# Performance work log

Measured on AMD Instinct MI355X. Metric: run time of the kernel, lower is better.

The kernel has to match this reference:

```python
import jax, jax.numpy as jnp
import numpy as np

SEQ_LEN, BATCH, HID, INP = 512, 256, 256, 256


def setup_inputs() -> dict:
    key = jax.random.key(0)
    ks = jax.random.split(key, 6)
    s = 1.0 / np.sqrt(HID)  # torch GRUCell init scale
    return {
        "carry": jnp.zeros((BATCH, HID), jnp.float32),
        "seq_inputs": jax.random.normal(ks[0], (SEQ_LEN, BATCH, INP), jnp.float32),
        "seq_resets": jax.random.randint(ks[1], (SEQ_LEN, BATCH), 0, 2, jnp.int32),
        "w_ih": jax.random.uniform(ks[2], (3 * HID, INP), jnp.float32, -s, s),
        "w_hh": jax.random.uniform(ks[3], (3 * HID, HID), jnp.float32, -s, s),
        "b_ih": jax.random.uniform(ks[4], (3 * HID,), jnp.float32, -s, s),
        "b_hh": jax.random.uniform(ks[5], (3 * HID,), jnp.float32, -s, s),
    }


def reference(carry, seq_inputs, seq_resets, w_ih, w_hh, b_ih, b_hh):
    # Precompute the input-side projection for all timesteps in one GEMM.
    gi_all = jnp.einsum('tbi,gi->tbg', seq_inputs, w_ih) + b_ih  # (T,B,3H)

    def step(h, xs):
        gi, reset_t = xs
        h = jnp.where(reset_t[:, None] > 0, jnp.zeros_like(h), h)
        gh = h @ w_hh.T + b_hh  # (B,3H)
        i_r, i_z, i_n = jnp.split(gi, 3, axis=1)
        h_r, h_z, h_n = jnp.split(gh, 3, axis=1)
        r = jax.nn.sigmoid(i_r + h_r)
        z = jax.nn.sigmoid(i_z + h_z)
        n = jnp.tanh(i_n + r * h_n)
        h_new = (1.0 - z) * n + z * h
        return h_new, h_new

    h_final, outputs = jax.lax.scan(step, carry, (gi_all, seq_resets))
    return h_final, outputs
```

## Files before the change

### kernel.cpp

```cpp
#include <hip/hip_runtime.h>
#include <hip/hip_bf16.h>
#include <hip/hip_fp16.h>


#define T_LEN 512
#define BATCH 256
#define HID   256

typedef __attribute__((ext_vector_type(8))) short s16x8;
typedef __attribute__((ext_vector_type(4))) float fx4;
typedef __attribute__((ext_vector_type(4))) unsigned short u16x4;

#define MFMA16 __builtin_amdgcn_mfma_f32_16x16x32_bf16

#define GATE_STRIDE 4096u
#define BLK_STRIDE  12288u
#define T_STRIDE    196608u

__device__ __forceinline__ unsigned short f2bf(float f) {
  union { float f; unsigned u; } v; v.f = f;
  unsigned r = v.u + 0x7fffu + ((v.u >> 16) & 1u);
  return (unsigned short)(r >> 16);
}

__device__ __forceinline__ s16x8 pack8(float4 a, float4 b) {
  s16x8 f;
  f[0] = (short)f2bf(a.x); f[1] = (short)f2bf(a.y);
  f[2] = (short)f2bf(a.z); f[3] = (short)f2bf(a.w);
  f[4] = (short)f2bf(b.x); f[5] = (short)f2bf(b.y);
  f[6] = (short)f2bf(b.z); f[7] = (short)f2bf(b.w);
  return f;
}

__device__ __forceinline__ void load_weights(const float* __restrict__ W,
                                             s16x8 (&wr)[2][2][8], char* Wlds,
                                             int tid, int wid, int col, int kgrp) {
#pragma unroll
  for (int n = 0; n < 2; ++n)
#pragma unroll
    for (int ht = 0; ht < 2; ++ht) {
      int g = n * 256 + (wid * 2 + ht) * 16 + col;
#pragma unroll
      for (int s8 = 0; s8 < 8; ++s8) {
        int k = s8 * 32 + kgrp * 8;
        const float4* p = (const float4*)(W + g * 256 + k);
        wr[n][ht][s8] = pack8(p[0], p[1]);
      }
    }
#pragma unroll
  for (int q = 0; q < 16; ++q) {
    int li = tid + q * 512;
    int wv = li >> 9, s8 = (li >> 6) & 7, l = li & 63;
    int g = 512 + wv * 16 + (l & 15);
    int k = s8 * 32 + (l >> 4) * 8;
    const float4* p = (const float4*)(W + g * 256 + k);
    *(s16x8*)(Wlds + li * 16) = pack8(p[0], p[1]);
  }
}

__device__ __forceinline__ void soft_barrier() {
  asm volatile("s_waitcnt lgkmcnt(0)" ::: "memory");
  __builtin_amdgcn_s_barrier();
  __builtin_amdgcn_sched_barrier(0);
  asm volatile("" ::: "memory");
}

__global__ __launch_bounds__(512, 2) void gi_proj_kernel(
    const float* __restrict__ X, const float* __restrict__ w_ih,
    const float* __restrict__ b_ih, const float* __restrict__ b_hh,
    __half* __restrict__ gi) {
  __shared__ __align__(16) char Wlds[131072];
  __shared__ __align__(16) char Ald[2][8192];

  const int tid = threadIdx.x;
  const int wid = tid >> 6, lane = tid & 63;
  const int col = lane & 15, kgrp = lane >> 4;

  s16x8 wr[2][2][8];
  load_weights(w_ih, wr, Wlds, tid, wid, col, kgrp);

  float bias[2][3];
#pragma unroll
  for (int ht = 0; ht < 2; ++ht) {
    int gb = (wid * 2 + ht) * 16 + col;
    bias[ht][0] = b_ih[gb]       + b_hh[gb];
    bias[ht][1] = b_ih[256 + gb] + b_hh[256 + gb];
    bias[ht][2] = b_ih[512 + gb];
  }

  const int srow = tid >> 5, sk = (tid & 31) * 8;
  const unsigned sbyte = ((unsigned)(srow * 512 + sk * 2)) ^ ((unsigned)(srow & 7) << 4);

  float4 xc0 = *(const float4*)(X + (size_t)(blockIdx.x * 16 + srow) * 256 + sk);
  float4 xc1 = *(const float4*)(X + (size_t)(blockIdx.x * 16 + srow) * 256 + sk + 4);

  int parity = 0;
  for (int chunk = blockIdx.x; chunk < (T_LEN * BATCH) / 16; chunk += 256) {
    char* ab = Ald[parity];
    {
      uint4 v;
      v.x = (unsigned)f2bf(xc0.x) | ((unsigned)f2bf(xc0.y) << 16);
      v.y = (unsigned)f2bf(xc0.z) | ((unsigned)f2bf(xc0.w) << 16);
      v.z = (unsigned)f2bf(xc1.x) | ((unsigned)f2bf(xc1.y) << 16);
      v.w = (unsigned)f2bf(xc1.z) | ((unsigned)f2bf(xc1.w) << 16);
      *(uint4*)(ab + sbyte) = v;
    }
    int nchunk = chunk + 256;
    if (nchunk < (T_LEN * BATCH) / 16) {
      xc0 = *(const float4*)(X + (size_t)(nchunk * 16 + srow) * 256 + sk);
      xc1 = *(const float4*)(X + (size_t)(nchunk * 16 + srow) * 256 + sk + 4);
    }
    soft_barrier();

    fx4 acc[2][3];
#pragma unroll
    for (int ht = 0; ht < 2; ++ht)
#pragma unroll
      for (int g = 0; g < 3; ++g)
        acc[ht][g] = (fx4){0.f, 0.f, 0.f, 0.f};

#pragma unroll
    for (int s8 = 0; s8 < 8; ++s8) {
      unsigned aoff = ((unsigned)(col * 512 + (s8 * 32 + kgrp * 8) * 2)) ^
                      ((unsigned)(col & 7) << 4);
      s16x8 af = *(const s16x8*)(ab + aoff);
#pragma unroll
      for (int ht = 0; ht < 2; ++ht) {
        s16x8 w2 = *(const s16x8*)(Wlds + (((wid * 2 + ht) * 8 + s8) * 64 + lane) * 16);
        acc[ht][0] = MFMA16(af, wr[0][ht][s8], acc[ht][0], 0, 0, 0);
        acc[ht][1] = MFMA16(af, wr[1][ht][s8], acc[ht][1], 0, 0, 0);
        acc[ht][2] = MFMA16(af, w2, acc[ht][2], 0, 0, 0);
      }
    }

#pragma unroll
    for (int ht = 0; ht < 2; ++ht) {
      __half* gb = gi + (size_t)chunk * BLK_STRIDE +
                   (unsigned)((wid * 2 + ht) * 16 + col) * 16 + kgrp * 4;
      u16x4 o0, o1, o2;
#pragma unroll
      for (int j = 0; j < 4; ++j) {
        o0[j] = __half_as_ushort(__float2half(acc[ht][0][j] + bias[ht][0]));
        o1[j] = __half_as_ushort(__float2half(acc[ht][1][j] + bias[ht][1]));
        o2[j] = __half_as_ushort(__float2half(acc[ht][2][j] + bias[ht][2]));
      }
      *(u16x4*)(gb) = o0;
      *(u16x4*)(gb + GATE_STRIDE) = o1;
      *(u16x4*)(gb + 2 * GATE_STRIDE) = o2;
    }
    parity ^= 1;
  }
}

__global__ __launch_bounds__(512, 2) void gru_scan_kernel(
    const float* __restrict__ carry, const __half* __restrict__ gi,
    const int* __restrict__ resets, const float* __restrict__ w_hh,
    const float* __restrict__ b_hh, float* __restrict__ out) {
  __shared__ __align__(16) char Wlds[131072];
  __shared__ __align__(16) char Ald[2][8192];
  __shared__ int lastreset[16];

  const int tid = threadIdx.x;
  const int wid = tid >> 6, lane = tid & 63;
  const int col = lane & 15, kgrp = lane >> 4;
  const int bid = blockIdx.x;
  const int bt = bid & 15, c = bid >> 4;
  const int b0 = bt * 16, t0 = c * 32, t1 = t0 + 32;
  const int hid0 = wid * 32 + col;

  s16x8 wr[2][2][8];
  load_weights(w_hh, wr, Wlds, tid, wid, col, kgrp);
  const float bhhn0 = b_hh[512 + hid0], bhhn1 = b_hh[512 + hid0 + 16];

  int s, useCarry;
  if (c == 0) {
    s = 0; useCarry = 1;
  } else {
    if (tid < 16) lastreset[tid] = -1;
    for (int base = t0 - 32;; base -= 32) {
      __syncthreads();
      int tt = base + (tid >> 4);
      if (tt >= 0 && tt < t0) {
        if (resets[tt * BATCH + b0 + (tid & 15)] != 0)
          atomicMax(&lastreset[tid & 15], tt);
      }
      __syncthreads();
      int mn = t0, all = 1;
#pragma unroll
      for (int i = 0; i < 16; ++i) {
        int v = lastreset[i];
        all &= (v >= 0) ? 1 : 0;
        mn = min(mn, v < 0 ? t0 : v);
      }
      if (all) { s = mn; useCarry = 0; break; }
      if (base <= 0) { s = 0; useCarry = 1; break; }
    }
  }

  {
    int row = tid >> 5, k = (tid & 31) * 8;
    int rst = resets[s * BATCH + b0 + row];
    float4 v0 = {0.f, 0.f, 0.f, 0.f}, v1 = v0;
    if (useCarry && !rst) {
      v0 = *(const float4*)(carry + (size_t)(b0 + row) * HID + k);
      v1 = *(const float4*)(carry + (size_t)(b0 + row) * HID + k + 4);
    }
    uint4 u;
    u.x = (unsigned)f2bf(v0.x) | ((unsigned)f2bf(v0.y) << 16);
    u.y = (unsigned)f2bf(v0.z) | ((unsigned)f2bf(v0.w) << 16);
    u.z = (unsigned)f2bf(v1.x) | ((unsigned)f2bf(v1.y) << 16);
    u.w = (unsigned)f2bf(v1.z) | ((unsigned)f2bf(v1.w) << 16);
    unsigned byteoff = ((unsigned)(row * 512 + k * 2)) ^ ((unsigned)(row & 7) << 4);
    *(uint4*)(Ald[0] + byteoff) = u;
  }
  float hprev[2][4];
#pragma unroll
  for (int ht = 0; ht < 2; ++ht)
#pragma unroll
    for (int j = 0; j < 4; ++j) {
      int b = kgrp * 4 + j;
      int rst = resets[s * BATCH + b0 + b];
      float hv = 0.f;
      if (useCarry && !rst) hv = carry[(size_t)(b0 + b) * HID + hid0 + ht * 16];
      hprev[ht][j] = hv;
    }
  __syncthreads();

  const __half* gp = gi + (size_t)(s * 16 + bt) * BLK_STRIDE + (unsigned)hid0 * 16 + kgrp * 4;
  float* op = out + 65536 + ((size_t)s * BATCH + b0 + kgrp * 4) * HID + hid0;
  const int* rbase = resets + b0 + kgrp * 4;

  u16x4 gC[2][3];
#pragma unroll
  for (int ht = 0; ht < 2; ++ht)
#pragma unroll
    for (int g = 0; g < 3; ++g)
      gC[ht][g] = *(const u16x4*)(gp + ht * 256u + g * GATE_STRIDE);
  int4 rnC = *(const int4*)(rbase + (size_t)min(s + 1, T_LEN - 1) * BATCH);

  for (int t = s; t < t1; ++t) {
    const bool more = (t + 1 < t1);
    const __half* gq = gp + (more ? T_STRIDE : 0u);
    u16x4 gN[2][3];
#pragma unroll
    for (int ht = 0; ht < 2; ++ht)
#pragma unroll
      for (int g = 0; g < 3; ++g)
        gN[ht][g] = *(const u16x4*)(gq + ht * 256u + g * GATE_STRIDE);
    int4 rnN = *(const int4*)(rbase + (size_t)min(t + 2, T_LEN - 1) * BATCH);

    const char* ab = Ald[(t - s) & 1];
    fx4 acc[2][3];
#pragma unroll
    for (int ht = 0; ht < 2; ++ht)
#pragma unroll
      for (int g = 0; g < 3; ++g)
        acc[ht][g] = (fx4){0.f, 0.f, 0.f, 0.f};

#pragma unroll
    for (int s8 = 0; s8 < 8; ++s8) {
      unsigned aoff = ((unsigned)(col * 512 + (s8 * 32 + kgrp * 8) * 2)) ^
                      ((unsigned)(col & 7) << 4);
      s16x8 af = *(const s16x8*)(ab + aoff);
#pragma unroll
      for (int ht = 0; ht < 2; ++ht) {
        s16x8 w2 = *(const s16x8*)(Wlds + (((wid * 2 + ht) * 8 + s8) * 64 + lane) * 16);
        acc[ht][0] = MFMA16(af, wr[0][ht][s8], acc[ht][0], 0, 0, 0);
        acc[ht][1] = MFMA16(af, wr[1][ht][s8], acc[ht][1], 0, 0, 0);
        acc[ht][2] = MFMA16(af, w2, acc[ht][2], 0, 0, 0);
      }
    }

    char* aw = (char*)Ald[((t - s) & 1) ^ 1];
    const bool wr_out = (t >= t0);
    const bool lastT  = (t + 1 >= T_LEN);
#pragma unroll
    for (int j = 0; j < 4; ++j) {
      int b = kgrp * 4 + j;
      int rj = (j == 0) ? rnC.x : (j == 1) ? rnC.y : (j == 2) ? rnC.z : rnC.w;
      if (lastT) rj = 0;
#pragma unroll
      for (int ht = 0; ht < 2; ++ht) {
        float pr = __half2float(__ushort_as_half(gC[ht][0][j])) + acc[ht][0][j];
        float pz = __half2float(__ushort_as_half(gC[ht][1][j])) + acc[ht][1][j];
        float r = __builtin_amdgcn_rcpf(1.f + __expf(-pr));
        float z = __builtin_amdgcn_rcpf(1.f + __expf(-pz));
        float pn = __half2float(__ushort_as_half(gC[ht][2][j])) +
                   r * (acc[ht][2][j] + (ht ? bhhn1 : bhhn0));
        float n = 1.f - 2.f * __builtin_amdgcn_rcpf(1.f + __expf(2.f * pn));
        float hnew = (1.f - z) * n + z * hprev[ht][j];
        if (wr_out) op[j * HID + ht * 16] = hnew;
        float hk = rj ? 0.f : hnew;
        hprev[ht][j] = hk;
        unsigned hoff = ((unsigned)(b * 512 + (hid0 + ht * 16) * 2)) ^
                        ((unsigned)(b & 7) << 4);
        *(unsigned short*)(aw + hoff) = f2bf(hk);
      }
    }

#pragma unroll
    for (int ht = 0; ht < 2; ++ht)
#pragma unroll
      for (int g = 0; g < 3; ++g)
        gC[ht][g] = gN[ht][g];
    rnC = rnN;
    gp = gq;
    op += 65536;
    soft_barrier();
  }

  if (c == 15) {
#pragma unroll
    for (int ht = 0; ht < 2; ++ht)
#pragma unroll
      for (int j = 0; j < 4; ++j)
        out[(size_t)(b0 + kgrp * 4 + j) * HID + hid0 + ht * 16] = hprev[ht][j];
  }
}

extern "C" void kernel_launch(void* const* d_in, const int* in_sizes, int n_in,
                              void* d_out, int out_size, void* d_ws, size_t ws_size,
                              hipStream_t stream) {
  const float* carry = (const float*)d_in[0];
  const float* X     = (const float*)d_in[1];
  const int*   rsts  = (const int*)d_in[2];
  const float* w_ih  = (const float*)d_in[3];
  const float* w_hh  = (const float*)d_in[4];
  const float* b_ih  = (const float*)d_in[5];
  const float* b_hh  = (const float*)d_in[6];
  float* out = (float*)d_out;

  const size_t gi_bytes = (size_t)T_LEN * BATCH * 3 * HID * sizeof(__half);
  if (ws_size < gi_bytes) return;
  __half* gi = (__half*)d_ws;

  gi_proj_kernel<<<256, 512, 0, stream>>>(X, w_ih, b_ih, b_hh, gi);
  gru_scan_kernel<<<256, 512, 0, stream>>>(carry, gi, rsts, w_hh, b_hh, out);
}
```

Baseline: 246.3 us.

## Hold 5 of 6 weight fragments in registers, halve LDS weights, vectorize gi layout

Five of the six per-wave weight fragments per gate/half-tile now live in registers, and only the n-gate second half-tile is staged in LDS. That cuts weight LDS from 128KB to 64KB and halves the per-step LDS weight reads. The gi intermediate layout becomes per-lane contiguous 8-halves, so both kernels use one 16-byte load/store per gate instead of two 8-byte ones. The reset prefetch is simplified to load within the step. The extra register pressure (40 vs 32 s16x8) risks spills, or lower occupancy under launch bounds of 512 threads x 2.

```diff
diff --git a/kernel.cpp b/kernel.cpp
--- a/kernel.cpp
+++ b/kernel.cpp
@@ -8,8 +8,8 @@
 #define HID   256
 
 typedef __attribute__((ext_vector_type(8))) short s16x8;
+typedef __attribute__((ext_vector_type(8))) unsigned short u16x8;
 typedef __attribute__((ext_vector_type(4))) float fx4;
-typedef __attribute__((ext_vector_type(4))) unsigned short u16x4;
 
 #define MFMA16 __builtin_amdgcn_mfma_f32_16x16x32_bf16
 
@@ -33,28 +33,29 @@
 }
 
 __device__ __forceinline__ void load_weights(const float* __restrict__ W,
-                                             s16x8 (&wr)[2][2][8], char* Wlds,
+                                             s16x8 (&wr)[5][8], char* Wl2,
                                              int tid, int wid, int col, int kgrp) {
 #pragma unroll
-  for (int n = 0; n < 2; ++n)
+  for (int g = 0; g < 3; ++g)
 #pragma unroll
     for (int ht = 0; ht < 2; ++ht) {
-      int g = n * 256 + (wid * 2 + ht) * 16 + col;
+      if (g == 2 && ht == 1) continue;
+      int row = g * 256 + (wid * 2 + ht) * 16 + col;
 #pragma unroll
       for (int s8 = 0; s8 < 8; ++s8) {
         int k = s8 * 32 + kgrp * 8;
-        const float4* p = (const float4*)(W + g * 256 + k);
-        wr[n][ht][s8] = pack8(p[0], p[1]);
-      }
-    }
-#pragma unroll
-  for (int q = 0; q < 16; ++q) {
+        const float4* p = (const float4*)(W + row * 256 + k);
+        wr[g * 2 + ht][s8] = pack8(p[0], p[1]);
+      }
+    }
+#pragma unroll
+  for (int q = 0; q < 8; ++q) {
     int li = tid + q * 512;
     int wv = li >> 9, s8 = (li >> 6) & 7, l = li & 63;
-    int g = 512 + wv * 16 + (l & 15);
+    int row = 512 + (wv * 2 + 1) * 16 + (l & 15);
     int k = s8 * 32 + (l >> 4) * 8;
-    const float4* p = (const float4*)(W + g * 256 + k);
-    *(s16x8*)(Wlds + li * 16) = pack8(p[0], p[1]);
+    const float4* p = (const float4*)(W + row * 256 + k);
+    *(s16x8*)(Wl2 + li * 16) = pack8(p[0], p[1]);
   }
 }
 
@@ -69,15 +70,15 @@
     const float* __restrict__ X, const float* __restrict__ w_ih,
     const float* __restrict__ b_ih, const float* __restrict__ b_hh,
     __half* __restrict__ gi) {
-  __shared__ __align__(16) char Wlds[131072];
+  __shared__ __align__(16) char Wl2[65536];
   __shared__ __align__(16) char Ald[2][8192];
 
   const int tid = threadIdx.x;
   const int wid = tid >> 6, lane = tid & 63;
   const int col = lane & 15, kgrp = lane >> 4;
 
-  s16x8 wr[2][2][8];
-  load_weights(w_ih, wr, Wlds, tid, wid, col, kgrp);
+  s16x8 wr[5][8];
+  load_weights(w_ih, wr, Wl2, tid, wid, col, kgrp);
 
   float bias[2][3];
 #pragma unroll
@@ -124,29 +125,25 @@
       unsigned aoff = ((unsigned)(col * 512 + (s8 * 32 + kgrp * 8) * 2)) ^
                       ((unsigned)(col & 7) << 4);
       s16x8 af = *(const s16x8*)(ab + aoff);
-#pragma unroll
-      for (int ht = 0; ht < 2; ++ht) {
-        s16x8 w2 = *(const s16x8*)(Wlds + (((wid * 2 + ht) * 8 + s8) * 64 + lane) * 16);
-        acc[ht][0] = MFMA16(af, wr[0][ht][s8], acc[ht][0], 0, 0, 0);
-        acc[ht][1] = MFMA16(af, wr[1][ht][s8], acc[ht][1], 0, 0, 0);
-        acc[ht][2] = MFMA16(af, w2, acc[ht][2], 0, 0, 0);
-      }
-    }
-
-#pragma unroll
-    for (int ht = 0; ht < 2; ++ht) {
-      __half* gb = gi + (size_t)chunk * BLK_STRIDE +
-                   (unsigned)((wid * 2 + ht) * 16 + col) * 16 + kgrp * 4;
-      u16x4 o0, o1, o2;
+      s16x8 w2 = *(const s16x8*)(Wl2 + ((wid * 8 + s8) * 64 + lane) * 16);
+      acc[0][0] = MFMA16(af, wr[0][s8], acc[0][0], 0, 0, 0);
+      acc[1][0] = MFMA16(af, wr[1][s8], acc[1][0], 0, 0, 0);
+      acc[0][1] = MFMA16(af, wr[2][s8], acc[0][1], 0, 0, 0);
+      acc[1][1] = MFMA16(af, wr[3][s8], acc[1][1], 0, 0, 0);
+      acc[0][2] = MFMA16(af, wr[4][s8], acc[0][2], 0, 0, 0);
+      acc[1][2] = MFMA16(af, w2, acc[1][2], 0, 0, 0);
+    }
+
+    __half* gb = gi + (size_t)chunk * BLK_STRIDE + (unsigned)(wid * 64 + lane) * 8;
+#pragma unroll
+    for (int g = 0; g < 3; ++g) {
+      u16x8 o;
 #pragma unroll
       for (int j = 0; j < 4; ++j) {
-        o0[j] = __half_as_ushort(__float2half(acc[ht][0][j] + bias[ht][0]));
-        o1[j] = __half_as_ushort(__float2half(acc[ht][1][j] + bias[ht][1]));
-        o2[j] = __half_as_ushort(__float2half(acc[ht][2][j] + bias[ht][2]));
-      }
-      *(u16x4*)(gb) = o0;
-      *(u16x4*)(gb + GATE_STRIDE) = o1;
-      *(u16x4*)(gb + 2 * GATE_STRIDE) = o2;
+        o[j]     = __half_as_ushort(__float2half(acc[0][g][j] + bias[0][g]));
+        o[4 + j] = __half_as_ushort(__float2half(acc[1][g][j] + bias[1][g]));
+      }
+      *(u16x8*)(gb + g * GATE_STRIDE) = o;
     }
     parity ^= 1;
   }
@@ -156,7 +153,7 @@
     const float* __restrict__ carry, const __half* __restrict__ gi,
     const int* __restrict__ resets, const float* __restrict__ w_hh,
     const float* __restrict__ b_hh, float* __restrict__ out) {
-  __shared__ __align__(16) char Wlds[131072];
+  __shared__ __align__(16) char Wl2[65536];
   __shared__ __align__(16) char Ald[2][8192];
   __shared__ int lastreset[16];
 
@@ -168,8 +165,8 @@
   const int b0 = bt * 16, t0 = c * 32, t1 = t0 + 32;
   const int hid0 = wid * 32 + col;
 
-  s16x8 wr[2][2][8];
-  load_weights(w_hh, wr, Wlds, tid, wid, col, kgrp);
+  s16x8 wr[5][8];
+  load_weights(w_hh, wr, Wl2, tid, wid, col, kgrp);
   const float bhhn0 = b_hh[512 + hid0], bhhn1 = b_hh[512 + hid0 + 16];
 
   int s, useCarry;
@@ -226,28 +223,23 @@
     }
   __syncthreads();
 
-  const __half* gp = gi + (size_t)(s * 16 + bt) * BLK_STRIDE + (unsigned)hid0 * 16 + kgrp * 4;
+  const __half* gp = gi + (size_t)(s * 16 + bt) * BLK_STRIDE + (unsigned)(wid * 64 + lane) * 8;
   float* op = out + 65536 + ((size_t)s * BATCH + b0 + kgrp * 4) * HID + hid0;
   const int* rbase = resets + b0 + kgrp * 4;
 
-  u16x4 gC[2][3];
-#pragma unroll
-  for (int ht = 0; ht < 2; ++ht)
+  u16x8 gC[3];
+#pragma unroll
+  for (int g = 0; g < 3; ++g)
+    gC[g] = *(const u16x8*)(gp + g * GATE_STRIDE);
+
+  for (int t = s; t < t1; ++t) {
+    int tn = t + 1 < T_LEN ? t + 1 : T_LEN - 1;
+    int4 rn = *(const int4*)(rbase + (size_t)tn * BATCH);
+    const __half* gq = gp + ((t + 1 < t1) ? T_STRIDE : 0u);
+    u16x8 gN[3];
 #pragma unroll
     for (int g = 0; g < 3; ++g)
-      gC[ht][g] = *(const u16x4*)(gp + ht * 256u + g * GATE_STRIDE);
-  int4 rnC = *(const int4*)(rbase + (size_t)min(s + 1, T_LEN - 1) * BATCH);
-
-  for (int t = s; t < t1; ++t) {
-    const bool more = (t + 1 < t1);
-    const __half* gq = gp + (more ? T_STRIDE : 0u);
-    u16x4 gN[2][3];
-#pragma unroll
-    for (int ht = 0; ht < 2; ++ht)
-#pragma unroll
-      for (int g = 0; g < 3; ++g)
-        gN[ht][g] = *(const u16x4*)(gq + ht * 256u + g * GATE_STRIDE);
-    int4 rnN = *(const int4*)(rbase + (size_t)min(t + 2, T_LEN - 1) * BATCH);
+      gN[g] = *(const u16x8*)(gq + g * GATE_STRIDE);
 
     const char* ab = Ald[(t - s) & 1];
     fx4 acc[2][3];
@@ -262,13 +254,13 @@
       unsigned aoff = ((unsigned)(col * 512 + (s8 * 32 + kgrp * 8) * 2)) ^
                       ((unsigned)(col & 7) << 4);
       s16x8 af = *(const s16x8*)(ab + aoff);
-#pragma unroll
-      for (int ht = 0; ht < 2; ++ht) {
-        s16x8 w2 = *(const s16x8*)(Wlds + (((wid * 2 + ht) * 8 + s8) * 64 + lane) * 16);
-        acc[ht][0] = MFMA16(af, wr[0][ht][s8], acc[ht][0], 0, 0, 0);
-        acc[ht][1] = MFMA16(af, wr[1][ht][s8], acc[ht][1], 0, 0, 0);
-        acc[ht][2] = MFMA16(af, w2, acc[ht][2], 0, 0, 0);
-      }
+      s16x8 w2 = *(const s16x8*)(Wl2 + ((wid * 8 + s8) * 64 + lane) * 16);
+      acc[0][0] = MFMA16(af, wr[0][s8], acc[0][0], 0, 0, 0);
+      acc[1][0] = MFMA16(af, wr[1][s8], acc[1][0], 0, 0, 0);
+      acc[0][1] = MFMA16(af, wr[2][s8], acc[0][1], 0, 0, 0);
+      acc[1][1] = MFMA16(af, wr[3][s8], acc[1][1], 0, 0, 0);
+      acc[0][2] = MFMA16(af, wr[4][s8], acc[0][2], 0, 0, 0);
+      acc[1][2] = MFMA16(af, w2, acc[1][2], 0, 0, 0);
     }
 
     char* aw = (char*)Ald[((t - s) & 1) ^ 1];
@@ -277,15 +269,15 @@
 #pragma unroll
     for (int j = 0; j < 4; ++j) {
       int b = kgrp * 4 + j;
-      int rj = (j == 0) ? rnC.x : (j == 1) ? rnC.y : (j == 2) ? rnC.z : rnC.w;
+      int rj = (j == 0) ? rn.x : (j == 1) ? rn.y : (j == 2) ? rn.z : rn.w;
       if (lastT) rj = 0;
 #pragma unroll
       for (int ht = 0; ht < 2; ++ht) {
-        float pr = __half2float(__ushort_as_half(gC[ht][0][j])) + acc[ht][0][j];
-        float pz = __half2float(__ushort_as_half(gC[ht][1][j])) + acc[ht][1][j];
+        float pr = __half2float(__ushort_as_half(gC[0][ht * 4 + j])) + acc[ht][0][j];
+        float pz = __half2float(__ushort_as_half(gC[1][ht * 4 + j])) + acc[ht][1][j];
         float r = __builtin_amdgcn_rcpf(1.f + __expf(-pr));
         float z = __builtin_amdgcn_rcpf(1.f + __expf(-pz));
-        float pn = __half2float(__ushort_as_half(gC[ht][2][j])) +
+        float pn = __half2float(__ushort_as_half(gC[2][ht * 4 + j])) +
                    r * (acc[ht][2][j] + (ht ? bhhn1 : bhhn0));
         float n = 1.f - 2.f * __builtin_amdgcn_rcpf(1.f + __expf(2.f * pn));
         float hnew = (1.f - z) * n + z * hprev[ht][j];
@@ -299,11 +291,7 @@
     }
 
 #pragma unroll
-    for (int ht = 0; ht < 2; ++ht)
-#pragma unroll
-      for (int g = 0; g < 3; ++g)
-        gC[ht][g] = gN[ht][g];
-    rnC = rnN;
+    for (int g = 0; g < 3; ++g) gC[g] = gN[g];
     gp = gq;
     op += 65536;
     soft_barrier();
```

After: 315.8 us. 1.28x slower.
